# Optimization experiments

Measured on AMD Instinct MI355X. Metric: run time of the kernel, lower is better.

## Reference

```python
import jax, jax.numpy as jnp
import numpy as np

L, H, D, V, T, B = 12, 12, 768, 50257, 1024, 2
HD = D // H


def _ln(x, w, b):
    m = jnp.mean(x, axis=-1, keepdims=True)
    v = jnp.var(x, axis=-1, keepdims=True)
    return (x - m) * jax.lax.rsqrt(v + 1e-5) * w + b


def setup_inputs() -> dict:
    key = jax.random.key(0)
    ks = jax.random.split(key, 8)
    def n(k, shape, std=0.02):
        return jax.random.normal(k, shape, jnp.float32) * std
    return dict(
        x=jax.random.randint(ks[0], (B, T), 0, V),
        wte=n(ks[1], (V, D), 0.01),
        wpe=n(ks[2], (T, D), 0.01),
        ln1_w=jnp.ones((L, D), jnp.float32), ln1_b=jnp.zeros((L, D), jnp.float32),
        qkv_w=n(ks[3], (L, D, 3 * D)), qkv_b=jnp.zeros((L, 3 * D), jnp.float32),
        proj_w=n(ks[4], (L, D, D)), proj_b=jnp.zeros((L, D), jnp.float32),
        ln2_w=jnp.ones((L, D), jnp.float32), ln2_b=jnp.zeros((L, D), jnp.float32),
        fc_w=n(ks[5], (L, D, 4 * D)), fc_b=jnp.zeros((L, 4 * D), jnp.float32),
        fcp_w=n(ks[6], (L, 4 * D, D)), fcp_b=jnp.zeros((L, D), jnp.float32),
        lnf_w=jnp.ones((D,), jnp.float32), lnf_b=jnp.zeros((D,), jnp.float32),
    )


def reference(x, wte, wpe, ln1_w, ln1_b, qkv_w, qkv_b, proj_w, proj_b,
              ln2_w, ln2_b, fc_w, fc_b, fcp_w, fcp_b, lnf_w, lnf_b):
    Bn, Tn = x.shape
    h = wte[x] + wpe[:Tn]                                   # [B,T,D]
    mask = jnp.tril(jnp.ones((Tn, Tn), bool))               # causal mask
    scale = 1.0 / np.sqrt(HD).astype(np.float32)

    def block(h, p):
        l1w, l1b, qw, qb, pw, pb, l2w, l2b, fw, fb, p2w, p2b = p
        a = _ln(h, l1w, l1b)
        qkv = a @ qw + qb                                    # [B,T,3D]
        q, k, v = jnp.split(qkv, 3, axis=-1)
        q = q.reshape(Bn, Tn, H, HD)
        k = k.reshape(Bn, Tn, H, HD)
        v = v.reshape(Bn, Tn, H, HD)
        att = jnp.einsum('bqhd,bkhd->bhqk', q, k) * scale    # [B,H,T,T]
        att = jnp.where(mask, att, -jnp.inf)
        att = jax.nn.softmax(att, axis=-1)
        y = jnp.einsum('bhqk,bkhd->bqhd', att, v).reshape(Bn, Tn, D)
        h = h + y @ pw + pb
        m = _ln(h, l2w, l2b)
        m = jax.nn.gelu(m @ fw + fb, approximate=True)       # tanh GELU
        h = h + m @ p2w + p2b
        return h, None

    h, _ = jax.lax.scan(block, h, (ln1_w, ln1_b, qkv_w, qkv_b, proj_w, proj_b,
                                   ln2_w, ln2_b, fc_w, fc_b, fcp_w, fcp_b))
    logits = _ln(h, lnf_w, lnf_b) @ wte.T                    # tied lm_head
    return logits
```

## Files before the change

### kernel.cpp

```cpp
#include <hip/hip_runtime.h>
#include <hip/hip_bf16.h>

typedef __hip_bfloat16 hbf16;
using bf16x8 = __attribute__((ext_vector_type(8))) __bf16;
using f32x4 = __attribute__((ext_vector_type(4))) float;

constexpr int Lc = 12, Hc = 12, Dc = 768, Vc = 50257, Tc = 1024, Bc = 2, HDc = 64;
constexpr int Mc = Bc * Tc;
constexpr int Vpad = 50304;

constexpr size_t SZ_Q = (size_t)3 * Dc * Dc;
constexpr size_t SZ_P = (size_t)Dc * Dc;
constexpr size_t SZ_F = (size_t)4 * Dc * Dc;
constexpr size_t SZ_FP = (size_t)4 * Dc * Dc;
constexpr size_t SZL = SZ_Q + SZ_P + SZ_F + SZ_FP;

#define GLD16(gp, lp)                                               \
    __builtin_amdgcn_global_load_lds(                               \
        (__attribute__((address_space(1))) void*)(void*)(gp),       \
        (__attribute__((address_space(3))) void*)(void*)(lp), 16, 0, 0)

__global__ void embed_kernel(const int* __restrict__ x, const float* __restrict__ wte,
                             const float* __restrict__ wpe, float* __restrict__ h) {
    int i = blockIdx.x * blockDim.x + threadIdx.x;
    if (i >= Mc * Dc) return;
    int m = i / Dc, d = i - m * Dc;
    int t = m % Tc;
    int tok = x[m];
    h[i] = wte[(size_t)tok * Dc + d] + wpe[(size_t)t * Dc + d];
}

__global__ __launch_bounds__(256) void ln_kernel(const float* __restrict__ x,
                                                 const float* __restrict__ w,
                                                 const float* __restrict__ b,
                                                 hbf16* __restrict__ out) {
    int wv = threadIdx.x >> 6, lane = threadIdx.x & 63;
    int row = blockIdx.x * 4 + wv;
    const float4* xr = (const float4*)(x + (size_t)row * Dc);
    float4 v[3];
    float s = 0.f, sq = 0.f;
#pragma unroll
    for (int i = 0; i < 3; i++) {
        v[i] = xr[i * 64 + lane];
        s += v[i].x + v[i].y + v[i].z + v[i].w;
        sq += v[i].x * v[i].x + v[i].y * v[i].y + v[i].z * v[i].z + v[i].w * v[i].w;
    }
#pragma unroll
    for (int o = 32; o > 0; o >>= 1) {
        s += __shfl_xor(s, o, 64);
        sq += __shfl_xor(sq, o, 64);
    }
    float mean = s * (1.f / Dc);
    float var = sq * (1.f / Dc) - mean * mean;
    float rstd = rsqrtf(var + 1e-5f);
#pragma unroll
    for (int i = 0; i < 3; i++) {
        int c = (i * 64 + lane) * 4;
        float4 wv4 = *(const float4*)(w + c);
        float4 bv4 = *(const float4*)(b + c);
        float r0 = (v[i].x - mean) * rstd * wv4.x + bv4.x;
        float r1 = (v[i].y - mean) * rstd * wv4.y + bv4.y;
        float r2 = (v[i].z - mean) * rstd * wv4.z + bv4.z;
        float r3 = (v[i].w - mean) * rstd * wv4.w + bv4.w;
        __bf16 q0 = (__bf16)r0, q1 = (__bf16)r1, q2 = (__bf16)r2, q3 = (__bf16)r3;
        ushort4 u;
        u.x = *(unsigned short*)&q0; u.y = *(unsigned short*)&q1;
        u.z = *(unsigned short*)&q2; u.w = *(unsigned short*)&q3;
        *(ushort4*)(out + (size_t)row * Dc + c) = u;
    }
}

__global__ __launch_bounds__(256) void transpose4_kernel(
    const float* __restrict__ s0, const float* __restrict__ s1,
    const float* __restrict__ s2, const float* __restrict__ s3,
    hbf16* __restrict__ d0, hbf16* __restrict__ d1,
    hbf16* __restrict__ d2, hbf16* __restrict__ d3) {
    int id = blockIdx.x;
    size_t lz = blockIdx.y;
    int bx, by, K, N;
    const float* W;
    hbf16* Wt;
    if (id < 1728)      { int t = id;        bx = t % 72; by = t / 72; K = 768;  N = 2304; W = s0 + lz * SZ_Q;  Wt = d0 + lz * SZL; }
    else if (id < 2304) { int t = id - 1728; bx = t % 24; by = t / 24; K = 768;  N = 768;  W = s1 + lz * SZ_P;  Wt = d1 + lz * SZL; }
    else if (id < 4608) { int t = id - 2304; bx = t % 96; by = t / 96; K = 768;  N = 3072; W = s2 + lz * SZ_F;  Wt = d2 + lz * SZL; }
    else                { int t = id - 4608; bx = t % 24; by = t / 24; K = 3072; N = 768;  W = s3 + lz * SZ_FP; Wt = d3 + lz * SZL; }

    __shared__ float tile[32][33];
    int n0 = bx * 32, k0 = by * 32;
    int tx = threadIdx.x & 31, ty = threadIdx.x >> 5;
#pragma unroll
    for (int i = 0; i < 4; i++) {
        int r = ty + i * 8;
        tile[r][tx] = W[(size_t)(k0 + r) * N + n0 + tx];
    }
    __syncthreads();
#pragma unroll
    for (int i = 0; i < 4; i++) {
        int r = ty + i * 8;
        Wt[(size_t)(n0 + r) * K + k0 + tx] = __float2bfloat16(tile[tx][r]);
    }
}

__global__ void convert_wte(const float* __restrict__ wte, hbf16* __restrict__ out) {
    size_t i4 = ((size_t)blockIdx.x * 256 + threadIdx.x) * 4;
    if (i4 >= (size_t)Vpad * Dc) return;
    if (i4 < (size_t)Vc * Dc) {
#pragma unroll
        for (int j = 0; j < 4; j++) out[i4 + j] = __float2bfloat16(wte[i4 + j]);
    } else {
#pragma unroll
        for (int j = 0; j < 4; j++) out[i4 + j] = __float2bfloat16(0.f);
    }
}

template <int EPI, bool OUTBF, int BN>
__global__ __launch_bounds__(256) void mm_kernel(const hbf16* __restrict__ A,
                                                 const hbf16* __restrict__ Bt,
                                                 const float* __restrict__ bias,
                                                 const float* __restrict__ resid,
                                                 void* __restrict__ Cout,
                                                 int M, int N, int K) {
    constexpr int NF = BN / 32;
    constexpr int NBI = BN / 32;
    __shared__ __bf16 As[128 * 64];
    __shared__ __bf16 Bs[BN * 64];
    int tid = threadIdx.x;
    int l = tid & 63, w = tid >> 6;
    int wr = w >> 1, wc = w & 1;

    int gx = gridDim.x, gy = gridDim.y;
    int nwg = gx * gy;
    int hwlin = blockIdx.y * gx + blockIdx.x;
    int wk = (hwlin & 7) * (nwg >> 3) + (hwlin >> 3);
    int m0 = (wk % gy) * 128;
    int n0 = (wk / gy) * BN;

    int sr = tid >> 3, sc = tid & 7;
    int scs = (sc ^ (sr & 7)) * 8;
    const hbf16* pA[4];
    __bf16* lA[4];
#pragma unroll
    for (int j = 0; j < 4; j++) {
        pA[j] = A + (size_t)(m0 + j * 32 + sr) * K + scs;
        lA[j] = As + j * 2048 + tid * 8;
    }
    const hbf16* pB[NBI];
    __bf16* lB[NBI];
#pragma unroll
    for (int j = 0; j < NBI; j++) {
        pB[j] = Bt + (size_t)(n0 + j * 32 + sr) * K + scs;
        lB[j] = Bs + j * 2048 + tid * 8;
    }

    int lr = l & 15, lg = l >> 4;
    int aoff[2][4], boff[2][NF];
#pragma unroll
    for (int kk = 0; kk < 2; kk++) {
        int ks = ((kk * 4 + lg) ^ (lr & 7)) * 8;
#pragma unroll
        for (int m = 0; m < 4; m++) aoff[kk][m] = (wr * 64 + m * 16 + lr) * 64 + ks;
#pragma unroll
        for (int n = 0; n < NF; n++) boff[kk][n] = (wc * (BN / 2) + n * 16 + lr) * 64 + ks;
    }

    f32x4 acc[4][NF] = {};

    for (int k0 = 0; k0 < K; k0 += 64) {
#pragma unroll
        for (int j = 0; j < 4; j++) {
            GLD16(pA[j], lA[j]);
            pA[j] += 64;
        }
#pragma unroll
        for (int j = 0; j < NBI; j++) {
            GLD16(pB[j], lB[j]);
            pB[j] += 64;
        }
        __syncthreads();
#pragma unroll
        for (int kk = 0; kk < 2; kk++) {
            bf16x8 af[4], bfr[NF];
#pragma unroll
            for (int m = 0; m < 4; m++) af[m] = *(const bf16x8*)&As[aoff[kk][m]];
#pragma unroll
            for (int n = 0; n < NF; n++) bfr[n] = *(const bf16x8*)&Bs[boff[kk][n]];
#pragma unroll
            for (int m = 0; m < 4; m++)
#pragma unroll
                for (int n = 0; n < NF; n++)
                    acc[m][n] = __builtin_amdgcn_mfma_f32_16x16x32_bf16(af[m], bfr[n], acc[m][n], 0, 0, 0);
        }
        __syncthreads();
    }

#pragma unroll
    for (int n = 0; n < NF; n++) {
        int col = n0 + wc * (BN / 2) + n * 16 + lr;
        bool cok = col < N;
        float bv = (bias && cok) ? bias[col] : 0.f;
#pragma unroll
        for (int m = 0; m < 4; m++) {
#pragma unroll
            for (int r = 0; r < 4; r++) {
                int row = m0 + wr * 64 + m * 16 + lg * 4 + r;
                if (!cok) continue;
                float v = acc[m][n][r] + bv;
                if (EPI == 1) v += resid[(size_t)row * N + col];
                if (EPI == 2) {
                    float x3 = v * v * v;
                    v = 0.5f * v * (1.f + tanhf(0.7978845608028654f * (v + 0.044715f * x3)));
                }
                if (OUTBF)
                    ((hbf16*)Cout)[(size_t)row * N + col] = __float2bfloat16(v);
                else
                    ((float*)Cout)[(size_t)row * N + col] = v;
            }
        }
    }
}

__global__ __launch_bounds__(512) void mm2_kernel(const hbf16* __restrict__ A,
                                                  const hbf16* __restrict__ Bt,
                                                  float* __restrict__ Cout,
                                                  int M, int N, int K) {
    __shared__ __bf16 As[2][256 * 32];
    __shared__ __bf16 Bs[2][128 * 32];
    int tid = threadIdx.x;
    int l = tid & 63, w = tid >> 6;
    int wr = w >> 1, wc = w & 1;

    int gx = gridDim.x, gy = gridDim.y;
    int nwg = gx * gy;
    int hwlin = blockIdx.y * gx + blockIdx.x;
    int wk = (hwlin & 7) * (nwg >> 3) + (hwlin >> 3);
    int m0 = (wk & 7) * 256;
    int n0 = (wk >> 3) * 128;

    int sr = tid >> 2, sc = tid & 3;
    int scs = (sc ^ (sr & 3)) * 8;
    const hbf16* gA0 = A + (size_t)(m0 + sr) * K + scs;
    const hbf16* gA1 = A + (size_t)(m0 + 128 + sr) * K + scs;
    const hbf16* gB = Bt + (size_t)(n0 + sr) * K + scs;

    auto stage = [&](int bi, int ko) {
        GLD16(gA0 + ko, &As[bi][tid * 8]);
        GLD16(gA1 + ko, &As[bi][4096 + tid * 8]);
        GLD16(gB + ko, &Bs[bi][tid * 8]);
    };

    int lr = l & 15, lg = l >> 4;
    int ksl = (lg ^ (lr & 3)) * 8;
    int aoff[4], boff[4];
#pragma unroll
    for (int m = 0; m < 4; m++) aoff[m] = (wr * 64 + m * 16 + lr) * 32 + ksl;
#pragma unroll
    for (int n = 0; n < 4; n++) boff[n] = (wc * 64 + n * 16 + lr) * 32 + ksl;

    f32x4 acc[4][4] = {};
    int nk = K / 32;

    stage(0, 0);
    __syncthreads();
    for (int t = 0; t < nk; ++t) {
        int cur = t & 1;
        if (t + 1 < nk) stage(cur ^ 1, (t + 1) * 32);
        bf16x8 af[4], bfr[4];
#pragma unroll
        for (int m = 0; m < 4; m++) af[m] = *(const bf16x8*)&As[cur][aoff[m]];
#pragma unroll
        for (int n = 0; n < 4; n++) bfr[n] = *(const bf16x8*)&Bs[cur][boff[n]];
#pragma unroll
        for (int m = 0; m < 4; m++)
#pragma unroll
            for (int n = 0; n < 4; n++)
                acc[m][n] = __builtin_amdgcn_mfma_f32_16x16x32_bf16(af[m], bfr[n], acc[m][n], 0, 0, 0);
        __syncthreads();
    }

#pragma unroll
    for (int n = 0; n < 4; n++) {
        int col = n0 + wc * 64 + n * 16 + lr;
        if (col >= N) continue;
#pragma unroll
        for (int m = 0; m < 4; m++) {
#pragma unroll
            for (int r = 0; r < 4; r++) {
                int row = m0 + wr * 64 + m * 16 + lg * 4 + r;
                Cout[(size_t)row * N + col] = acc[m][n][r];
            }
        }
    }
}

__global__ __launch_bounds__(256) void fattn_kernel(const hbf16* __restrict__ qkv,
                                                    hbf16* __restrict__ y) {
    int qt = gridDim.x - 1 - blockIdx.x;
    int h = blockIdx.y, b = blockIdx.z;
    int q0 = qt * 64;
    int tid = threadIdx.x;
    int l = tid & 63, w = tid >> 6;
    int li = l & 15, lg = l >> 4;
    constexpr int RS = 3 * Dc;
    constexpr int PST = 72;
    constexpr int VST = 72;
    constexpr float SCL = 0.125f * 1.44269504f;
    constexpr float THR = 11.5f;

    __shared__ __bf16 K_lds[2][64 * 64];
    __shared__ __bf16 Vt[2][64 * VST];
    __shared__ __bf16 P_lds[4][16 * PST];

    bf16x8 qf[2];
    {
        const hbf16* qp = qkv + (size_t)(b * Tc + q0 + w * 16 + li) * RS + h * HDc + lg * 8;
        qf[0] = *(const bf16x8*)qp;
        qf[1] = *(const bf16x8*)(qp + 32);
    }

    int krow0 = tid >> 3, krow1 = 32 + (tid >> 3);
    int ks8 = tid & 7;
    int kc0 = (ks8 ^ (krow0 & 7)) * 8;
    int kc1 = (ks8 ^ (krow1 & 7)) * 8;
    const hbf16* kbase = qkv + (size_t)(b * Tc) * RS + Dc + h * HDc;

    int jp = (tid >> 3) * 2;
    int db = (tid & 7) * 8;
    const hbf16* vbase = qkv + (size_t)(b * Tc) * RS + 2 * Dc + h * HDc;

    int koff[2][4];
#pragma unroll
    for (int ks = 0; ks < 2; ks++)
#pragma unroll
        for (int n = 0; n < 4; n++)
            koff[ks][n] = (n * 16 + li) * 64 + (((ks * 4 + lg) ^ (li & 7)) * 8);

    f32x4 acc_o[4] = {};
    float m_run = -1e30f, l_run = 0.f;

    bf16x8 vr0, vr1;
    {
        const hbf16* vp = vbase + (size_t)jp * RS + db;
        vr0 = *(const bf16x8*)vp;
        vr1 = *(const bf16x8*)(vp + RS);
        GLD16(kbase + (size_t)krow0 * RS + kc0, &K_lds[0][tid * 8]);
        GLD16(kbase + (size_t)krow1 * RS + kc1, &K_lds[0][2048 + tid * 8]);
    }
#pragma unroll
    for (int i = 0; i < 8; i++) {
        __bf16 a0 = vr0[i], a1 = vr1[i];
        unsigned u = (unsigned)*(unsigned short*)&a0 | ((unsigned)*(unsigned short*)&a1 << 16);
        *(unsigned*)&Vt[0][(db + i) * VST + jp] = u;
    }

    int cur = 0;
    for (int jt = 0; jt <= qt; jt++) {
        int jn0 = (jt < qt) ? (jt + 1) * 64 : 0;

        asm volatile("s_waitcnt lgkmcnt(0)" ::: "memory");
        __builtin_amdgcn_s_barrier();

        {
            const hbf16* vp = vbase + (size_t)(jn0 + jp) * RS + db;
            vr0 = *(const bf16x8*)vp;
            vr1 = *(const bf16x8*)(vp + RS);
            GLD16(kbase + (size_t)(jn0 + krow0) * RS + kc0, &K_lds[cur ^ 1][tid * 8]);
            GLD16(kbase + (size_t)(jn0 + krow1) * RS + kc1, &K_lds[cur ^ 1][2048 + tid * 8]);
        }

        asm volatile("s_waitcnt vmcnt(4)" ::: "memory");
        __builtin_amdgcn_sched_barrier(0);

        f32x4 s[4] = {};
#pragma unroll
        for (int ks = 0; ks < 2; ks++)
#pragma unroll
            for (int n = 0; n < 4; n++) {
                bf16x8 kf = *(const bf16x8*)&K_lds[cur][koff[ks][n]];
                s[n] = __builtin_amdgcn_mfma_f32_16x16x32_bf16(kf, qf[ks], s[n], 0, 0, 0);
            }
#pragma unroll
        for (int n = 0; n < 4; n++)
#pragma unroll
            for (int r = 0; r < 4; r++) s[n][r] *= SCL;

        if (jt == qt) {
            int qloc = w * 16 + li;
#pragma unroll
            for (int n = 0; n < 4; n++)
#pragma unroll
                for (int r = 0; r < 4; r++)
                    if (n * 16 + lg * 4 + r > qloc) s[n][r] = -1e30f;
        }

        float mx = -1e30f;
#pragma unroll
        for (int n = 0; n < 4; n++)
#pragma unroll
            for (int r = 0; r < 4; r++) mx = fmaxf(mx, s[n][r]);
        mx = fmaxf(mx, __shfl_xor(mx, 16, 64));
        mx = fmaxf(mx, __shfl_xor(mx, 32, 64));

        bool dfr = __all(mx - m_run <= THR);
        float sclq = 1.f;
        if (!dfr) {
            float mnew = fmaxf(m_run, mx);
            sclq = exp2f(m_run - mnew);
            m_run = mnew;
        }
        float rs = 0.f;
#pragma unroll
        for (int n = 0; n < 4; n++)
#pragma unroll
            for (int r = 0; r < 4; r++) {
                float pv = exp2f(s[n][r] - m_run);
                s[n][r] = pv;
                rs += pv;
            }
        rs += __shfl_xor(rs, 16, 64);
        rs += __shfl_xor(rs, 32, 64);
        l_run = (dfr ? l_run : l_run * sclq) + rs;

#pragma unroll
        for (int n = 0; n < 4; n++)
#pragma unroll
            for (int r = 0; r < 4; r += 2) {
                __bf16 b0 = (__bf16)s[n][r], b1 = (__bf16)s[n][r + 1];
                unsigned u = (unsigned)*(unsigned short*)&b0 |
                             ((unsigned)*(unsigned short*)&b1 << 16);
                *(unsigned*)&P_lds[w][li * PST + n * 16 + lg * 4 + r] = u;
            }
        bf16x8 pa0 = *(const bf16x8*)&P_lds[w][li * PST + lg * 8];
        bf16x8 pa1 = *(const bf16x8*)&P_lds[w][li * PST + 32 + lg * 8];

        if (!dfr) {
#pragma unroll
            for (int r = 0; r < 4; r++) {
                float sr_ = __shfl(sclq, (l & 48) | (lg * 4 + r), 64);
#pragma unroll
                for (int n2 = 0; n2 < 4; n2++) acc_o[n2][r] *= sr_;
            }
        }

#pragma unroll
        for (int n2 = 0; n2 < 4; n2++) {
            bf16x8 vf0 = *(const bf16x8*)&Vt[cur][(n2 * 16 + li) * VST + lg * 8];
            bf16x8 vf1 = *(const bf16x8*)&Vt[cur][(n2 * 16 + li) * VST + 32 + lg * 8];
            acc_o[n2] = __builtin_amdgcn_mfma_f32_16x16x32_bf16(pa0, vf0, acc_o[n2], 0, 0, 0);
            acc_o[n2] = __builtin_amdgcn_mfma_f32_16x16x32_bf16(pa1, vf1, acc_o[n2], 0, 0, 0);
        }

#pragma unroll
        for (int i = 0; i < 8; i++) {
            __bf16 a0 = vr0[i], a1 = vr1[i];
            unsigned u = (unsigned)*(unsigned short*)&a0 | ((unsigned)*(unsigned short*)&a1 << 16);
            *(unsigned*)&Vt[cur ^ 1][(db + i) * VST + jp] = u;
        }
        cur ^= 1;
    }

#pragma unroll
    for (int r = 0; r < 4; r++) {
        float lv = __shfl(l_run, (l & 48) | (lg * 4 + r), 64);
        float rcp = 1.f / lv;
        int row = q0 + w * 16 + lg * 4 + r;
#pragma unroll
        for (int n2 = 0; n2 < 4; n2++)
            y[(size_t)(b * Tc + row) * Dc + h * HDc + n2 * 16 + li] =
                __float2bfloat16(acc_o[n2][r] * rcp);
    }
}

extern "C" void kernel_launch(void* const* d_in, const int* in_sizes, int n_in,
                              void* d_out, int out_size, void* d_ws, size_t ws_size,
                              hipStream_t stream) {
    const int* x = (const int*)d_in[0];
    const float* wte = (const float*)d_in[1];
    const float* wpe = (const float*)d_in[2];
    const float* ln1w = (const float*)d_in[3];
    const float* ln1b = (const float*)d_in[4];
    const float* qkvw = (const float*)d_in[5];
    const float* qkvb = (const float*)d_in[6];
    const float* projw = (const float*)d_in[7];
    const float* projb = (const float*)d_in[8];
    const float* ln2w = (const float*)d_in[9];
    const float* ln2b = (const float*)d_in[10];
    const float* fcw = (const float*)d_in[11];
    const float* fcb = (const float*)d_in[12];
    const float* fcpw = (const float*)d_in[13];
    const float* fcpb = (const float*)d_in[14];
    const float* lnfw = (const float*)d_in[15];
    const float* lnfb = (const float*)d_in[16];

    char* p = (char*)d_ws;
    float* h = (float*)p;     p += (size_t)Mc * Dc * 4;
    hbf16* qkv = (hbf16*)p;   p += (size_t)Mc * 3 * Dc * 2;
    hbf16* a = (hbf16*)p;     p += (size_t)Mc * Dc * 2;
    hbf16* y = (hbf16*)p;     p += (size_t)Mc * Dc * 2;
    hbf16* mlp = (hbf16*)p;   p += (size_t)Mc * 4 * Dc * 2;
    hbf16* wte_b = (hbf16*)p; p += (size_t)Vpad * Dc * 2;
    hbf16* wtr = (hbf16*)p;
    size_t used = (size_t)((char*)wtr - (char*)d_ws);
    bool all_mode = (ws_size - used) >= (size_t)Lc * SZL * 2;

    embed_kernel<<<(Mc * Dc + 255) / 256, 256, 0, stream>>>(x, wte, wpe, h);
    convert_wte<<<((size_t)Vpad * Dc / 4 + 255) / 256, 256, 0, stream>>>(wte, wte_b);

    if (all_mode) {
        transpose4_kernel<<<dim3(6912, Lc), 256, 0, stream>>>(
            qkvw, projw, fcw, fcpw,
            wtr, wtr + SZ_Q, wtr + SZ_Q + SZ_P, wtr + SZ_Q + SZ_P + SZ_F);
    }

    for (int l = 0; l < Lc; l++) {
        hbf16* base = wtr + (all_mode ? (size_t)l * SZL : 0);
        hbf16* wq_t = base;
        hbf16* wp_t = base + SZ_Q;
        hbf16* wf_t = base + SZ_Q + SZ_P;
        hbf16* wfp_t = base + SZ_Q + SZ_P + SZ_F;
        if (!all_mode) {
            transpose4_kernel<<<dim3(6912, 1), 256, 0, stream>>>(
                qkvw + (size_t)l * SZ_Q, projw + (size_t)l * SZ_P,
                fcw + (size_t)l * SZ_F, fcpw + (size_t)l * SZ_FP,
                wq_t, wp_t, wf_t, wfp_t);
        }

        ln_kernel<<<Mc / 4, 256, 0, stream>>>(h, ln1w + (size_t)l * Dc, ln1b + (size_t)l * Dc, a);
        mm_kernel<0, true, 128><<<dim3(3 * Dc / 128, Mc / 128), 256, 0, stream>>>(
            a, wq_t, qkvb + (size_t)l * 3 * Dc, nullptr, qkv, Mc, 3 * Dc, Dc);
        fattn_kernel<<<dim3(Tc / 64, Hc, Bc), 256, 0, stream>>>(qkv, y);
        mm_kernel<1, false, 64><<<dim3(Dc / 64, Mc / 128), 256, 0, stream>>>(
            y, wp_t, projb + (size_t)l * Dc, h, h, Mc, Dc, Dc);
        ln_kernel<<<Mc / 4, 256, 0, stream>>>(h, ln2w + (size_t)l * Dc, ln2b + (size_t)l * Dc, a);
        mm_kernel<2, true, 128><<<dim3(4 * Dc / 128, Mc / 128), 256, 0, stream>>>(
            a, wf_t, fcb + (size_t)l * 4 * Dc, nullptr, mlp, Mc, 4 * Dc, Dc);
        mm_kernel<1, false, 64><<<dim3(Dc / 64, Mc / 128), 256, 0, stream>>>(
            mlp, wfp_t, fcpb + (size_t)l * Dc, h, h, Mc, Dc, 4 * Dc);
    }

    ln_kernel<<<Mc / 4, 256, 0, stream>>>(h, lnfw, lnfb, a);
    mm2_kernel<<<dim3(Vpad / 128, Mc / 256), 512, 0, stream>>>(
        a, wte_b, (float*)d_out, Mc, Vc, Dc);
}
```

Before: 2.391 ms.

## Replace double-buffered K=32 staging with single-buffered K=64 tiles in mm2 kernel

The lm_head GEMM kernel now stages a 64-wide K slice into one LDS buffer per iteration instead of double-buffering 32-wide slices. The XOR swizzle is widened to 8 chunks. This halves the number of loop iterations and barriers per K and gives each barrier two MFMA sub-steps. In exchange it gives up the prefetch overlap between global loads and compute, since loads and compute are now serialized within each iteration.

```diff
diff --git a/kernel.cpp b/kernel.cpp
--- a/kernel.cpp
+++ b/kernel.cpp
@@ -223,8 +223,8 @@
                                                   const hbf16* __restrict__ Bt,
                                                   float* __restrict__ Cout,
                                                   int M, int N, int K) {
-    __shared__ __bf16 As[2][256 * 32];
-    __shared__ __bf16 Bs[2][128 * 32];
+    __shared__ __bf16 As[256 * 64];
+    __shared__ __bf16 Bs[128 * 64];
     int tid = threadIdx.x;
     int l = tid & 63, w = tid >> 6;
     int wr = w >> 1, wc = w & 1;
@@ -236,44 +236,61 @@
     int m0 = (wk & 7) * 256;
     int n0 = (wk >> 3) * 128;
 
-    int sr = tid >> 2, sc = tid & 3;
-    int scs = (sc ^ (sr & 3)) * 8;
-    const hbf16* gA0 = A + (size_t)(m0 + sr) * K + scs;
-    const hbf16* gA1 = A + (size_t)(m0 + 128 + sr) * K + scs;
-    const hbf16* gB = Bt + (size_t)(n0 + sr) * K + scs;
-
-    auto stage = [&](int bi, int ko) {
-        GLD16(gA0 + ko, &As[bi][tid * 8]);
-        GLD16(gA1 + ko, &As[bi][4096 + tid * 8]);
-        GLD16(gB + ko, &Bs[bi][tid * 8]);
-    };
+    int sr = tid >> 3, sc = tid & 7;
+    int scs = (sc ^ (sr & 7)) * 8;
+    const hbf16* pA[4];
+    __bf16* lA[4];
+#pragma unroll
+    for (int j = 0; j < 4; j++) {
+        pA[j] = A + (size_t)(m0 + j * 64 + sr) * K + scs;
+        lA[j] = As + j * 4096 + tid * 8;
+    }
+    const hbf16* pB[2];
+    __bf16* lB[2];
+#pragma unroll
+    for (int j = 0; j < 2; j++) {
+        pB[j] = Bt + (size_t)(n0 + j * 64 + sr) * K + scs;
+        lB[j] = Bs + j * 4096 + tid * 8;
+    }
 
     int lr = l & 15, lg = l >> 4;
-    int ksl = (lg ^ (lr & 3)) * 8;
-    int aoff[4], boff[4];
-#pragma unroll
-    for (int m = 0; m < 4; m++) aoff[m] = (wr * 64 + m * 16 + lr) * 32 + ksl;
-#pragma unroll
-    for (int n = 0; n < 4; n++) boff[n] = (wc * 64 + n * 16 + lr) * 32 + ksl;
+    int aoff[2][4], boff[2][4];
+#pragma unroll
+    for (int kk = 0; kk < 2; kk++) {
+        int ks = ((kk * 4 + lg) ^ (lr & 7)) * 8;
+#pragma unroll
+        for (int m = 0; m < 4; m++) aoff[kk][m] = (wr * 64 + m * 16 + lr) * 64 + ks;
+#pragma unroll
+        for (int n = 0; n < 4; n++) boff[kk][n] = (wc * 64 + n * 16 + lr) * 64 + ks;
+    }
 
     f32x4 acc[4][4] = {};
-    int nk = K / 32;
-
-    stage(0, 0);
-    __syncthreads();
-    for (int t = 0; t < nk; ++t) {
-        int cur = t & 1;
-        if (t + 1 < nk) stage(cur ^ 1, (t + 1) * 32);
-        bf16x8 af[4], bfr[4];
-#pragma unroll
-        for (int m = 0; m < 4; m++) af[m] = *(const bf16x8*)&As[cur][aoff[m]];
-#pragma unroll
-        for (int n = 0; n < 4; n++) bfr[n] = *(const bf16x8*)&Bs[cur][boff[n]];
-#pragma unroll
-        for (int m = 0; m < 4; m++)
-#pragma unroll
-            for (int n = 0; n < 4; n++)
-                acc[m][n] = __builtin_amdgcn_mfma_f32_16x16x32_bf16(af[m], bfr[n], acc[m][n], 0, 0, 0);
+
+    for (int k0 = 0; k0 < K; k0 += 64) {
+#pragma unroll
+        for (int j = 0; j < 4; j++) {
+            GLD16(pA[j], lA[j]);
+            pA[j] += 64;
+        }
+#pragma unroll
+        for (int j = 0; j < 2; j++) {
+            GLD16(pB[j], lB[j]);
+            pB[j] += 64;
+        }
+        __syncthreads();
+#pragma unroll
+        for (int kk = 0; kk < 2; kk++) {
+            bf16x8 af[4], bfr[4];
+#pragma unroll
+            for (int m = 0; m < 4; m++) af[m] = *(const bf16x8*)&As[aoff[kk][m]];
+#pragma unroll
+            for (int n = 0; n < 4; n++) bfr[n] = *(const bf16x8*)&Bs[boff[kk][n]];
+#pragma unroll
+            for (int m = 0; m < 4; m++)
+#pragma unroll
+                for (int n = 0; n < 4; n++)
+                    acc[m][n] = __builtin_amdgcn_mfma_f32_16x16x32_bf16(af[m], bfr[n], acc[m][n], 0, 0, 0);
+        }
         __syncthreads();
     }
 
```

Measured after the change: 2.371 ms. No clear change (-0.8%).
